# Performance work log

Measured on AMD Instinct MI355X. Metric: run time of the kernel, lower is better.

The kernel has to match this reference:

```python
import jax, jax.numpy as jnp
import numpy as np

NUM_HEADS = 16
D_K = 8  # == n_qubits


def setup_inputs() -> dict:
    key = jax.random.key(0)
    k1, k2, k3 = jax.random.split(key, 3)
    x = jax.random.normal(k1, (4, 2048, 128), dtype=jnp.float32)
    # trainable RX angles, one per qubit (tq.RX has_params=True)
    theta = jax.random.normal(k2, (D_K,), dtype=jnp.float32)
    # out_proj: Linear(embed_dim, embed_dim, bias=False)
    w_out = jax.random.normal(k3, (128, 128), dtype=jnp.float32) * (1.0 / np.sqrt(128.0))
    return {"x": x, "theta": theta, "w_out": w_out}


def quantum_features(x, theta):
    # x: [b, s, e]. Per head of size d_k: encode RX(x_i), trainable RX(theta_i)
    # (composes to RX(x_i + theta_i)), CNOT ladder [i, i+1], measure PauliZ.
    # Heisenberg picture: Z_w -> Z_0...Z_w, so <Z_w> = prod_{i<=w} cos(x_i + theta_i).
    b, s, e = x.shape
    heads = x.reshape(b, s, NUM_HEADS, D_K)
    return jnp.cumprod(jnp.cos(heads + theta), axis=-1)  # [b, s, h, d_k]


def reference(x, theta, w_out):
    b, s, e = x.shape
    # q == k == v: same shared q_layer applied to the same x three times.
    qkv = quantum_features(x, theta)            # [b, s, h, d_k]
    q = qkv.transpose(0, 2, 1, 3)               # [b, h, s, d_k]
    scores = jnp.einsum('bhqd,bhkd->bhqk', q, q) / np.sqrt(D_K)
    attn = jax.nn.softmax(scores, axis=-1)      # dropout is identity at eval
    out = jnp.einsum('bhqk,bhkd->bhqd', attn, q)
    out = out.transpose(0, 2, 1, 3).reshape(b, s, e)
    return out @ w_out.T
```

## Files before the change

### kernel.cpp

```cpp
#include <hip/hip_runtime.h>

#define BATCH 4
#define SEQ   2048
#define EMB   128
#define NH    16
#define DK    8

#define QSCALE 0.510069726f

typedef _Float16 v2h __attribute__((ext_vector_type(2)));
typedef _Float16 v4h __attribute__((ext_vector_type(4)));
typedef __fp16   v2fp __attribute__((ext_vector_type(2)));
typedef float    v4f __attribute__((ext_vector_type(4)));

#define CHUNK  512
#define NCHUNK (SEQ / CHUNK)
#define VTP    520

__launch_bounds__(256, 6)
__global__ void attn_kernel(const float* __restrict__ x,
                            const float* __restrict__ theta,
                            _Float16* __restrict__ Ah ) {
  __shared__ __align__(16) _Float16 Kl[CHUNK * 8];
  __shared__ __align__(16) _Float16 VT[16][VTP];

  const int tid  = threadIdx.x;
  const int L    = tid & 63;
  const int quad = L >> 4;
  const int ln   = L & 15;
  const int wv   = tid >> 6;
  const int bh     = blockIdx.x >> 4;
  const int qchunk = blockIdx.x & 15;
  const int qb     = qchunk * 128 + wv * 32;
  const int b = bh >> 4;
  const int h = bh & 15;

  float th[DK];
#pragma unroll
  for (int i = 0; i < DK; ++i) th[i] = theta[i];

  for (int i = tid; i < 8 * VTP / 4; i += 256) {
    v4h v = (i < VTP / 4) ? (v4h){(_Float16)1.f, (_Float16)1.f,
                                  (_Float16)1.f, (_Float16)1.f}
                          : (v4h){0, 0, 0, 0};
    *(v4h*)(&VT[8][0] + i * 4) = v;
  }

  const int c0 = qchunk >> 2;
  const float* xb = x + (size_t)b * SEQ * EMB + h * DK;

  float4 pa0, pa1, pb0, pb1;
  {
    const float* xp = xb + (size_t)(c0 * CHUNK + tid) * EMB;
    pa0 = *(const float4*)(xp);
    pa1 = *(const float4*)(xp + 4);
    pb0 = *(const float4*)(xp + 256 * EMB);
    pb1 = *(const float4*)(xp + 256 * EMB + 4);
  }

  v4h qf[2] = {{0, 0, 0, 0}, {0, 0, 0, 0}};
  v4f acc[2];
  acc[0] = (v4f){0.f, 0.f, 0.f, 0.f};
  acc[1] = (v4f){0.f, 0.f, 0.f, 0.f};
  const v4f zf = (v4f){0.f, 0.f, 0.f, 0.f};

  for (int cc = 0; cc < NCHUNK; ++cc) {
    if (cc) __syncthreads();

    {
      float r0[8], r1[8];
      r0[0] = __cosf(pa0.x + th[0]);
      r0[1] = r0[0] * __cosf(pa0.y + th[1]);
      r0[2] = r0[1] * __cosf(pa0.z + th[2]);
      r0[3] = r0[2] * __cosf(pa0.w + th[3]);
      r0[4] = r0[3] * __cosf(pa1.x + th[4]);
      r0[5] = r0[4] * __cosf(pa1.y + th[5]);
      r0[6] = r0[5] * __cosf(pa1.z + th[6]);
      r0[7] = r0[6] * __cosf(pa1.w + th[7]);
      r1[0] = __cosf(pb0.x + th[0]);
      r1[1] = r1[0] * __cosf(pb0.y + th[1]);
      r1[2] = r1[1] * __cosf(pb0.z + th[2]);
      r1[3] = r1[2] * __cosf(pb0.w + th[3]);
      r1[4] = r1[3] * __cosf(pb1.x + th[4]);
      r1[5] = r1[4] * __cosf(pb1.y + th[5]);
      r1[6] = r1[5] * __cosf(pb1.z + th[6]);
      r1[7] = r1[6] * __cosf(pb1.w + th[7]);

      _Float16 h0[8], h1[8];
#pragma unroll
      for (int i = 0; i < 8; ++i) { h0[i] = (_Float16)r0[i]; h1[i] = (_Float16)r1[i]; }

      union { v4h v[2]; float4 f; } u0, u1;
      u0.v[0] = (v4h){h0[0], h0[1], h0[2], h0[3]};
      u0.v[1] = (v4h){h0[4], h0[5], h0[6], h0[7]};
      u1.v[0] = (v4h){h1[0], h1[1], h1[2], h1[3]};
      u1.v[1] = (v4h){h1[4], h1[5], h1[6], h1[7]};
      *(float4*)&Kl[tid * 8]         = u0.f;
      *(float4*)&Kl[(tid + 256) * 8] = u1.f;

#pragma unroll
      for (int d = 0; d < 8; ++d) {
        VT[d][tid]       = h0[d];
        VT[d][tid + 256] = h1[d];
      }
    }
    __syncthreads();

    if (cc + 1 < NCHUNK) {
      const int cn = (c0 + cc + 1) & (NCHUNK - 1);
      const float* xp = xb + (size_t)(cn * CHUNK + tid) * EMB;
      pa0 = *(const float4*)(xp);
      pa1 = *(const float4*)(xp + 4);
      pb0 = *(const float4*)(xp + 256 * EMB);
      pb1 = *(const float4*)(xp + 256 * EMB + 4);
    }

    if (cc == 0) {
      const v4h qsc = {(_Float16)QSCALE, (_Float16)QSCALE,
                       (_Float16)QSCALE, (_Float16)QSCALE};
      const int lbase = qb - c0 * CHUNK + ln;
      if (quad < 2) {
        qf[0] = *(const v4h*)&Kl[(lbase)      * 8 + quad * 4] * qsc;
        qf[1] = *(const v4h*)&Kl[(lbase + 16) * 8 + quad * 4] * qsc;
      }
    }

#pragma unroll 4
    for (int t16 = 0; t16 < CHUNK / 16; ++t16) {
      const v4h kf = *(const v4h*)&Kl[(t16 * 16 + ln) * 8 + (quad & 1) * 4];
      const v4h vt = *(const v4h*)&VT[ln][t16 * 16 + quad * 4];
#pragma unroll
      for (int t = 0; t < 2; ++t) {
        const v4f s = __builtin_amdgcn_mfma_f32_16x16x16f16(kf, qf[t], zf, 0, 0, 0);
        union { v2fp p[2]; v4h v; } pk;
        pk.p[0] = __builtin_amdgcn_cvt_pkrtz(__builtin_amdgcn_exp2f(s[0]),
                                             __builtin_amdgcn_exp2f(s[1]));
        pk.p[1] = __builtin_amdgcn_cvt_pkrtz(__builtin_amdgcn_exp2f(s[2]),
                                             __builtin_amdgcn_exp2f(s[3]));
        acc[t] = __builtin_amdgcn_mfma_f32_16x16x16f16(vt, pk.v, acc[t], 0, 0, 0);
      }
    }
  }

#pragma unroll
  for (int t = 0; t < 2; ++t) {
    const float den = __shfl(acc[t][0], 32 + ln, 64);
    const float inv = 1.0f / den;
    if (quad < 2) {
      const int qrow = qb + t * 16 + ln;
      v4h o = {(_Float16)(acc[t][0] * inv), (_Float16)(acc[t][1] * inv),
               (_Float16)(acc[t][2] * inv), (_Float16)(acc[t][3] * inv)};
      *(v4h*)(Ah + ((size_t)b * SEQ + qrow) * EMB + h * DK + quad * 4) = o;
    }
  }
}

__launch_bounds__(256, 4)
__global__ void proj_kernel(const _Float16* __restrict__ Ah,
                            const float* __restrict__ W,
                            float* __restrict__ out) {
  __shared__ __align__(16) _Float16 Ahs[64][136];
  __shared__ __align__(16) _Float16 Whs[64][136];

  const int tid  = threadIdx.x;
  const int L    = tid & 63;
  const int wv   = tid >> 6;
  const int quad = L >> 4;
  const int ln   = L & 15;
  const int rowbase = blockIdx.x * 64;
  const int colbase = blockIdx.y * 64;

#pragma unroll
  for (int it = 0; it < 4; ++it) {
    const int idx = it * 256 + tid;
    const int r  = idx >> 4;
    const int c8 = idx & 15;
    *(uint4*)&Ahs[r][c8 * 8] =
        *(const uint4*)(Ah + (size_t)(rowbase + r) * EMB + c8 * 8);
  }
#pragma unroll
  for (int it = 0; it < 8; ++it) {
    const int idx = it * 256 + tid;
    const int n  = idx >> 5;
    const int c4 = idx & 31;
    const float4 w = *(const float4*)(W + (size_t)(colbase + n) * EMB + c4 * 4);
    v4h wh = {(_Float16)w.x, (_Float16)w.y, (_Float16)w.z, (_Float16)w.w};
    *(v4h*)&Whs[n][c4 * 4] = wh;
  }
  __syncthreads();

  v4f acc[4];
#pragma unroll
  for (int nt = 0; nt < 4; ++nt) acc[nt] = (v4f){0.f, 0.f, 0.f, 0.f};

#pragma unroll
  for (int k8 = 0; k8 < 8; ++k8) {
    const v4h af = *(const v4h*)&Ahs[wv * 16 + ln][k8 * 16 + quad * 4];
#pragma unroll
    for (int nt = 0; nt < 4; ++nt) {
      const v4h bf = *(const v4h*)&Whs[nt * 16 + ln][k8 * 16 + quad * 4];
      acc[nt] = __builtin_amdgcn_mfma_f32_16x16x16f16(af, bf, acc[nt], 0, 0, 0);
    }
  }

#pragma unroll
  for (int nt = 0; nt < 4; ++nt) {
    const int col = colbase + nt * 16 + ln;
#pragma unroll
    for (int r = 0; r < 4; ++r) {
      out[(size_t)(rowbase + wv * 16 + quad * 4 + r) * EMB + col] = acc[nt][r];
    }
  }
}

extern "C" void kernel_launch(void* const* d_in, const int* in_sizes, int n_in,
                              void* d_out, int out_size, void* d_ws, size_t ws_size,
                              hipStream_t stream) {
  const float* x     = (const float*)d_in[0];
  const float* theta = (const float*)d_in[1];
  const float* w_out = (const float*)d_in[2];
  float* out = (float*)d_out;

  _Float16* Ah = (_Float16*)d_ws;

  attn_kernel<<<dim3(1024), dim3(256), 0, stream>>>(x, theta, Ah);

  proj_kernel<<<dim3((BATCH * SEQ) / 64, 2), dim3(256), 0, stream>>>(Ah, w_out, out);
}
```

Measured before the change: 95.95 us.

## Switch attention inner loop to 32x32x16 MFMA with permuted V layout

Replaces the pairs of 16x16x16 f16 MFMAs per query tile with a single 32x32x16 MFMA for scores and two 32x32x16 MFMAs for the P·V accumulation, covering 32 queries per wave at once. To match the operand layout of the larger instruction, V^T columns are written to LDS with a bit-permuted key index, and a row of ones supplies the softmax denominator. The goal is fewer MFMA issues and LDS loads per key. In exchange, the accumulator grows to 16 floats per lane and the launch-bounds occupancy hint is lowered from 6 to 4.

```diff
diff --git a/kernel.cpp b/kernel.cpp
--- a/kernel.cpp
+++ b/kernel.cpp
@@ -8,27 +8,28 @@
 
 #define QSCALE 0.510069726f
 
-typedef _Float16 v2h __attribute__((ext_vector_type(2)));
-typedef _Float16 v4h __attribute__((ext_vector_type(4)));
+typedef _Float16 v4h  __attribute__((ext_vector_type(4)));
+typedef _Float16 v8h  __attribute__((ext_vector_type(8)));
 typedef __fp16   v2fp __attribute__((ext_vector_type(2)));
-typedef float    v4f __attribute__((ext_vector_type(4)));
+typedef float    v4f  __attribute__((ext_vector_type(4)));
+typedef float    v16f __attribute__((ext_vector_type(16)));
 
 #define CHUNK  512
-#define NCHUNK (SEQ / CHUNK)
+#define NCH    (SEQ / CHUNK)
 #define VTP    520
 
-__launch_bounds__(256, 6)
+__launch_bounds__(256, 4)
 __global__ void attn_kernel(const float* __restrict__ x,
                             const float* __restrict__ theta,
                             _Float16* __restrict__ Ah ) {
   __shared__ __align__(16) _Float16 Kl[CHUNK * 8];
-  __shared__ __align__(16) _Float16 VT[16][VTP];
-
-  const int tid  = threadIdx.x;
-  const int L    = tid & 63;
-  const int quad = L >> 4;
-  const int ln   = L & 15;
-  const int wv   = tid >> 6;
+  __shared__ __align__(16) _Float16 VT[10][VTP];
+
+  const int tid = threadIdx.x;
+  const int L   = tid & 63;
+  const int ln  = L & 31;
+  const int hf  = L >> 5;
+  const int wv  = tid >> 6;
   const int bh     = blockIdx.x >> 4;
   const int qchunk = blockIdx.x & 15;
   const int qb     = qchunk * 128 + wv * 32;
@@ -39,14 +40,13 @@
 #pragma unroll
   for (int i = 0; i < DK; ++i) th[i] = theta[i];
 
-  for (int i = tid; i < 8 * VTP / 4; i += 256) {
-    v4h v = (i < VTP / 4) ? (v4h){(_Float16)1.f, (_Float16)1.f,
-                                  (_Float16)1.f, (_Float16)1.f}
-                          : (v4h){0, 0, 0, 0};
-    *(v4h*)(&VT[8][0] + i * 4) = v;
+  for (int i = tid; i < VTP; i += 256) {
+    VT[8][i] = (_Float16)1.0f;
+    VT[9][i] = (_Float16)0.0f;
   }
 
   const int c0 = qchunk >> 2;
+  const int mrow = (ln < 9) ? ln : 9;
   const float* xb = x + (size_t)b * SEQ * EMB + h * DK;
 
   float4 pa0, pa1, pb0, pb1;
@@ -58,13 +58,15 @@
     pb1 = *(const float4*)(xp + 256 * EMB + 4);
   }
 
-  v4h qf[2] = {{0, 0, 0, 0}, {0, 0, 0, 0}};
-  v4f acc[2];
-  acc[0] = (v4f){0.f, 0.f, 0.f, 0.f};
-  acc[1] = (v4f){0.f, 0.f, 0.f, 0.f};
-  const v4f zf = (v4f){0.f, 0.f, 0.f, 0.f};
-
-  for (int cc = 0; cc < NCHUNK; ++cc) {
+  v8h qf = {0, 0, 0, 0, 0, 0, 0, 0};
+  v16f acc;
+#pragma unroll
+  for (int i = 0; i < 16; ++i) acc[i] = 0.f;
+  v16f zf;
+#pragma unroll
+  for (int i = 0; i < 16; ++i) zf[i] = 0.f;
+
+  for (int cc = 0; cc < NCH; ++cc) {
     if (cc) __syncthreads();
 
     {
@@ -98,16 +100,19 @@
       *(float4*)&Kl[tid * 8]         = u0.f;
       *(float4*)&Kl[(tid + 256) * 8] = u1.f;
 
+      const int j0 = tid, j1 = tid + 256;
+      const int col0 = (j0 & ~15) | (j0 & 3) | ((j0 & 4) << 1) | ((j0 & 8) >> 1);
+      const int col1 = (j1 & ~15) | (j1 & 3) | ((j1 & 4) << 1) | ((j1 & 8) >> 1);
 #pragma unroll
       for (int d = 0; d < 8; ++d) {
-        VT[d][tid]       = h0[d];
-        VT[d][tid + 256] = h1[d];
+        VT[d][col0] = h0[d];
+        VT[d][col1] = h1[d];
       }
     }
     __syncthreads();
 
-    if (cc + 1 < NCHUNK) {
-      const int cn = (c0 + cc + 1) & (NCHUNK - 1);
+    if (cc + 1 < NCH) {
+      const int cn = (c0 + cc + 1) & (NCH - 1);
       const float* xp = xb + (size_t)(cn * CHUNK + tid) * EMB;
       pa0 = *(const float4*)(xp);
       pa1 = *(const float4*)(xp + 4);
@@ -115,43 +120,41 @@
       pb1 = *(const float4*)(xp + 256 * EMB + 4);
     }
 
-    if (cc == 0) {
-      const v4h qsc = {(_Float16)QSCALE, (_Float16)QSCALE,
-                       (_Float16)QSCALE, (_Float16)QSCALE};
-      const int lbase = qb - c0 * CHUNK + ln;
-      if (quad < 2) {
-        qf[0] = *(const v4h*)&Kl[(lbase)      * 8 + quad * 4] * qsc;
-        qf[1] = *(const v4h*)&Kl[(lbase + 16) * 8 + quad * 4] * qsc;
+    if (cc == 0 && hf == 0) {
+      const int ql = (qchunk & 3) * 128 + wv * 32 + ln;
+      v8h qv = *(const v8h*)&Kl[ql * 8];
+      const _Float16 qs = (_Float16)QSCALE;
+      const v8h qsc = {qs, qs, qs, qs, qs, qs, qs, qs};
+      qf = qv * qsc;
+    }
+
+    for (int kb = 0; kb < CHUNK / 32; ++kb) {
+      const v8h kf = *(const v8h*)&Kl[(kb * 32 + ln) * 8];
+      const v16f s = __builtin_amdgcn_mfma_f32_32x32x16_f16(kf, qf, zf, 0, 0, 0);
+      union { v2fp p[4]; v8h v; } p0, p1;
+#pragma unroll
+      for (int i = 0; i < 4; ++i) {
+        p0.p[i] = __builtin_amdgcn_cvt_pkrtz(
+            __builtin_amdgcn_exp2f(s[2 * i]),
+            __builtin_amdgcn_exp2f(s[2 * i + 1]));
+        p1.p[i] = __builtin_amdgcn_cvt_pkrtz(
+            __builtin_amdgcn_exp2f(s[8 + 2 * i]),
+            __builtin_amdgcn_exp2f(s[8 + 2 * i + 1]));
       }
-    }
-
-#pragma unroll 4
-    for (int t16 = 0; t16 < CHUNK / 16; ++t16) {
-      const v4h kf = *(const v4h*)&Kl[(t16 * 16 + ln) * 8 + (quad & 1) * 4];
-      const v4h vt = *(const v4h*)&VT[ln][t16 * 16 + quad * 4];
-#pragma unroll
-      for (int t = 0; t < 2; ++t) {
-        const v4f s = __builtin_amdgcn_mfma_f32_16x16x16f16(kf, qf[t], zf, 0, 0, 0);
-        union { v2fp p[2]; v4h v; } pk;
-        pk.p[0] = __builtin_amdgcn_cvt_pkrtz(__builtin_amdgcn_exp2f(s[0]),
-                                             __builtin_amdgcn_exp2f(s[1]));
-        pk.p[1] = __builtin_amdgcn_cvt_pkrtz(__builtin_amdgcn_exp2f(s[2]),
-                                             __builtin_amdgcn_exp2f(s[3]));
-        acc[t] = __builtin_amdgcn_mfma_f32_16x16x16f16(vt, pk.v, acc[t], 0, 0, 0);
-      }
-    }
-  }
-
-#pragma unroll
-  for (int t = 0; t < 2; ++t) {
-    const float den = __shfl(acc[t][0], 32 + ln, 64);
+      const v8h vt0 = *(const v8h*)&VT[mrow][kb * 32 + hf * 8];
+      const v8h vt1 = *(const v8h*)&VT[mrow][kb * 32 + 16 + hf * 8];
+      acc = __builtin_amdgcn_mfma_f32_32x32x16_f16(vt0, p0.v, acc, 0, 0, 0);
+      acc = __builtin_amdgcn_mfma_f32_32x32x16_f16(vt1, p1.v, acc, 0, 0, 0);
+    }
+  }
+
+  {
+    const float den = __shfl(acc[4], ln, 64);
     const float inv = 1.0f / den;
-    if (quad < 2) {
-      const int qrow = qb + t * 16 + ln;
-      v4h o = {(_Float16)(acc[t][0] * inv), (_Float16)(acc[t][1] * inv),
-               (_Float16)(acc[t][2] * inv), (_Float16)(acc[t][3] * inv)};
-      *(v4h*)(Ah + ((size_t)b * SEQ + qrow) * EMB + h * DK + quad * 4) = o;
-    }
+    const int qrow = qb + ln;
+    v4h o = {(_Float16)(acc[0] * inv), (_Float16)(acc[1] * inv),
+             (_Float16)(acc[2] * inv), (_Float16)(acc[3] * inv)};
+    *(v4h*)(Ah + ((size_t)b * SEQ + qrow) * EMB + h * DK + hf * 4) = o;
   }
 }
 
```

New measurement: 94.73 us. About the same (-1.3%).
